# Kernel tuning notes

Measured on AMD Instinct MI355X. Metric: run time of the kernel, lower is better.

## Reference

```python
import jax, jax.numpy as jnp
import numpy as np

L, H = 6, 8          # depth, heads
DM, DH, M = 512, 64, 256  # d_model, d_head, nb random features
EPS = 1e-4


def sinusoidal_pe(n, d, dtype):
    pos = jnp.arange(n, dtype=jnp.float32)[:, None]
    div = jnp.exp(jnp.arange(0, d, 2, dtype=jnp.float32) * (-(np.log(10000.0) / d)))
    pe = jnp.zeros((n, d), jnp.float32)
    pe = pe.at[:, 0::2].set(jnp.sin(pos * div))
    pe = pe.at[:, 1::2].set(jnp.cos(pos * div))
    return pe.astype(dtype)


def layer_norm(x, g, b, eps=1e-5):
    mu = jnp.mean(x, -1, keepdims=True)
    var = jnp.mean(jnp.square(x - mu), -1, keepdims=True)
    return (x - mu) * jax.lax.rsqrt(var + eps) * g + b


def softmax_features(x, proj, is_query):
    # FAVOR+ positive softmax-kernel features. x: [b,h,n,dh], proj: [m,dh]
    dn = DH ** -0.25
    xd = x * dn
    u = jnp.einsum('bhnd,md->bhnm', xd, proj)            # [b,h,n,m]
    diag = 0.5 * jnp.sum(xd * xd, -1, keepdims=True)      # ||x||^2/2 (normalized)
    if is_query:
        stab = jnp.max(u, axis=-1, keepdims=True)
    else:
        stab = jnp.max(u, axis=(-2, -1), keepdims=True)
    return (M ** -0.5) * (jnp.exp(u - diag - stab) + EPS)


def split_heads(t, b, n):
    return t.reshape(b, n, H, DH).transpose(0, 2, 1, 3)   # [b,h,n,dh]


def reference(x, proj, ln1_g, ln1_b, wq, wk, wv, wo, bo, ln2_g, ln2_b, w1, b1, w2, b2):
    b, n, d = x.shape
    x = x + sinusoidal_pe(n, d, x.dtype)[None]
    for i in range(L):
        # --- FAVOR+ linear attention (pre-norm) ---
        h = layer_norm(x, ln1_g[i], ln1_b[i])
        q = split_heads(h @ wq[i], b, n)
        k = split_heads(h @ wk[i], b, n)
        v = split_heads(h @ wv[i], b, n)
        qp = softmax_features(q, proj[i], True)           # [b,h,n,m]
        kp = softmax_features(k, proj[i], False)
        ksum = jnp.sum(kp, axis=2)                         # [b,h,m]
        d_inv = 1.0 / jnp.einsum('bhnm,bhm->bhn', qp, ksum)
        ctx = jnp.einsum('bhnm,bhnd->bhmd', kp, v)         # [b,h,m,dh]
        o = jnp.einsum('bhnm,bhmd->bhnd', qp, ctx) * d_inv[..., None]
        o = o.transpose(0, 2, 1, 3).reshape(b, n, DM)
        x = x + o @ wo[i] + bo[i]
        # --- feed-forward (pre-norm, GELU) ---
        h = layer_norm(x, ln2_g[i], ln2_b[i])
        x = x + jax.nn.gelu(h @ w1[i] + b1[i], approximate=False) @ w2[i] + b2[i]
    return x


def setup_inputs() -> dict:
    key = jax.random.key(0)
    ks = jax.random.split(key, 9)
    s_in = DM ** -0.5
    s_ff = (4 * DM) ** -0.5
    return {
        'x':     jax.random.normal(ks[0], (8, 2048, DM), jnp.float32),
        'proj':  jax.random.normal(ks[1], (L, M, DH), jnp.float32),
        'ln1_g': jnp.ones((L, DM), jnp.float32),
        'ln1_b': jnp.zeros((L, DM), jnp.float32),
        'wq':    jax.random.normal(ks[2], (L, DM, DM), jnp.float32) * s_in,
        'wk':    jax.random.normal(ks[3], (L, DM, DM), jnp.float32) * s_in,
        'wv':    jax.random.normal(ks[4], (L, DM, DM), jnp.float32) * s_in,
        'wo':    jax.random.normal(ks[5], (L, DM, DM), jnp.float32) * s_in,
        'bo':    jnp.zeros((L, DM), jnp.float32),
        'ln2_g': jnp.ones((L, DM), jnp.float32),
        'ln2_b': jnp.zeros((L, DM), jnp.float32),
        'w1':    jax.random.normal(ks[6], (L, DM, 4 * DM), jnp.float32) * s_in,
        'b1':    jnp.zeros((L, 4 * DM), jnp.float32),
        'w2':    jax.random.normal(ks[7], (L, 4 * DM, DM), jnp.float32) * s_ff,
        'b2':    jnp.zeros((L, DM), jnp.float32),
    }
```

## Files before the change

kernel.cpp:

```cpp
#include <hip/hip_runtime.h>
#include <math.h>

#define LNUM 6
#define HNUM 8
#define DMODEL 512
#define DHEAD 64
#define MFEAT 256
#define BATCH 8
#define SEQ 2048
#define TOK (BATCH*SEQ)
#define BHN (BATCH*HNUM)
#define DFF 2048
#define EPSF 1e-4f
#define LN_EPS 1e-5f
#define DNRM 0.35355339059327373f
#define SMF 0.0625f

typedef unsigned short u16;
typedef __attribute__((ext_vector_type(8))) short bf16x8;
typedef __attribute__((ext_vector_type(4))) float f32x4;
#define MFMA16(a,b,c) __builtin_amdgcn_mfma_f32_16x16x32_bf16(a,b,c,0,0,0)

#define GLOAD16(g,l) __builtin_amdgcn_global_load_lds( \
    (const __attribute__((address_space(1))) void*)(g), \
    (__attribute__((address_space(3))) void*)(l), 16, 0, 0)

__device__ __forceinline__ u16 f2bf(float f){
  unsigned int u = __float_as_uint(f);
  u = (u + 0x7fffu + ((u >> 16) & 1u)) >> 16;
  return (u16)u;
}
__device__ __forceinline__ float bf2f(u16 s){
  return __uint_as_float(((unsigned int)s) << 16);
}
__device__ __forceinline__ void atomicMaxF(float* addr, float val){
  if(val >= 0.f) atomicMax((int*)addr, __float_as_int(val));
  else           atomicMin((unsigned int*)addr, __float_as_uint(val));
}
__device__ __forceinline__ float fast_gelu(float z){
  float g2 = z*(1.5957691216f + 0.07135481628f*z*z);
  return z / (1.0f + __expf(-g2));
}

__global__ void k_addpe(const float* __restrict__ x, float* __restrict__ xo){
  int idx = blockIdx.x*256 + threadIdx.x;
  int d = idx & (DMODEL-1);
  int n = (idx >> 9) & (SEQ-1);
  int j = d >> 1;
  float freq = expf((float)(2*j) * (-9.210340371976184f / (float)DMODEL));
  float ang = (float)n * freq;
  float pe = (d & 1) ? cosf(ang) : sinf(ang);
  xo[idx] = x[idx] + pe;
}

__global__ void k_ln(const float* __restrict__ x, const float* __restrict__ g,
                     const float* __restrict__ bv, u16* __restrict__ out){
  __shared__ float sred[8];
  int t = blockIdx.x, tid = threadIdx.x;
  const float2 v = ((const float2*)(x + (size_t)t*DMODEL))[tid];
  float s = v.x + v.y;
  #pragma unroll
  for(int o=32;o;o>>=1) s += __shfl_down(s,o);
  if((tid&63)==0) sred[tid>>6] = s;
  __syncthreads();
  if(tid==0) sred[4] = (sred[0]+sred[1]+sred[2]+sred[3]) * (1.0f/DMODEL);
  __syncthreads();
  float mu = sred[4];
  float dx = v.x - mu, dy = v.y - mu;
  float s2 = dx*dx + dy*dy;
  #pragma unroll
  for(int o=32;o;o>>=1) s2 += __shfl_down(s2,o);
  if((tid&63)==0) sred[tid>>6] = s2;
  __syncthreads();
  if(tid==0) sred[5] = rsqrtf((sred[0]+sred[1]+sred[2]+sred[3])*(1.0f/DMODEL) + LN_EPS);
  __syncthreads();
  float rs = sred[5];
  const float2 gg = ((const float2*)g)[tid];
  const float2 bb = ((const float2*)bv)[tid];
  ushort2 o2; o2.x = f2bf(dx*rs*gg.x + bb.x); o2.y = f2bf(dy*rs*gg.y + bb.y);
  ((ushort2*)(out + (size_t)t*DMODEL))[tid] = o2;
}

__global__ void k_pcvt(const float* __restrict__ p, u16* __restrict__ pb){
  int i = blockIdx.x*256 + threadIdx.x;
  pb[i] = f2bf(p[i]);
}

__global__ void k_wcvt_all(const float* __restrict__ wq, const float* __restrict__ wk,
                           const float* __restrict__ wv, const float* __restrict__ wo,
                           const float* __restrict__ w1, const float* __restrict__ w2,
                           u16* __restrict__ wqT, u16* __restrict__ wkT,
                           u16* __restrict__ wvT, u16* __restrict__ woT,
                           u16* __restrict__ w1T, u16* __restrict__ w2T,
                           float* __restrict__ ksum, float* __restrict__ kmax){
  int bid = blockIdx.x;
  if(bid >= 768){
    int i = (bid-768)*256 + threadIdx.x;
    ksum[i] = 0.f;
    if(i < BHN) kmax[i] = -INFINITY;
    return;
  }
  const float* src; u16* dst; int K, N, bx, by;
  if(bid < 256){
    int which = bid >> 6, sub = bid & 63;
    src = which==0 ? wq : which==1 ? wk : which==2 ? wv : wo;
    dst = which==0 ? wqT : which==1 ? wkT : which==2 ? wvT : woT;
    K = 512; N = 512; bx = sub & 7; by = sub >> 3;
  } else if(bid < 512){
    int sub = bid - 256; src = w1; dst = w1T; K = 512; N = 2048; bx = sub & 31; by = sub >> 5;
  } else {
    int sub = bid - 512; src = w2; dst = w2T; K = 2048; N = 512; bx = sub & 7; by = sub >> 3;
  }
  __shared__ float sm[64][65];
  int kt = by*64, nt = bx*64;
  int t = threadIdx.x, c = t & 63, r4 = t >> 6;
  #pragma unroll
  for(int i=0;i<16;i++){
    int kl = i*4 + r4;
    sm[kl][c] = src[(size_t)(kt+kl)*N + nt + c];
  }
  __syncthreads();
  #pragma unroll
  for(int i=0;i<16;i++){
    int nl = i*4 + r4;
    dst[(size_t)(nt+nl)*K + kt + c] = f2bf(sm[c][nl]);
  }
}

template<int EPI>
__global__ __launch_bounds__(256,4)
void k_mm(const u16* __restrict__ A, const u16* __restrict__ Bt,
          const float* __restrict__ bias, void* __restrict__ Cv,
          int Nc, int K){
  __shared__ u16 As[2][128*32];
  __shared__ u16 Bs[2][128*32];
  int tid = threadIdx.x;
  int w = tid >> 6, lane = tid & 63;
  int wr = w >> 1, wc = w & 1;
  int hi = lane >> 4, li = lane & 15;
  int row0 = blockIdx.y*128, col0 = blockIdx.x*128;
  int lr = lane >> 2;
  int cs = (lane & 3) ^ ((lane >> 3) & 3);
  const u16* gA = A  + (size_t)(row0 + w*16 + lr)*K + cs*8;
  const u16* gB = Bt + (size_t)(col0 + w*16 + lr)*K + cs*8;
  int rb = li*32 + ((hi ^ ((li>>1)&3))<<3);
  f32x4 acc[4][4] = {};

#define STAGE_MM(b,k0) { \
    GLOAD16(gA + (k0),                &As[b][(w*16)*32]);      \
    GLOAD16(gA + (size_t)64*K + (k0), &As[b][(64+w*16)*32]);   \
    GLOAD16(gB + (k0),                &Bs[b][(w*16)*32]);      \
    GLOAD16(gB + (size_t)64*K + (k0), &Bs[b][(64+w*16)*32]); }

  int nk = K >> 5;
  STAGE_MM(0, 0)
  STAGE_MM(1, 32)
  for(int t=0; t<nk; ++t){
    __builtin_amdgcn_sched_barrier(0);
    if(t+1 < nk){ asm volatile("s_waitcnt vmcnt(4)"); }
    else        { asm volatile("s_waitcnt vmcnt(0)"); }
    __builtin_amdgcn_s_barrier();
    __builtin_amdgcn_sched_barrier(0);
    const u16* pa = &As[t&1][0];
    const u16* pb = &Bs[t&1][0];
    bf16x8 bfr[4];
    #pragma unroll
    for(int q=0;q<4;q++) bfr[q] = *(const bf16x8*)&pb[rb + wc*2048 + q*512];
    #pragma unroll
    for(int i2=0;i2<4;i2++){
      bf16x8 a = *(const bf16x8*)&pa[rb + wr*2048 + i2*512];
      #pragma unroll
      for(int j2=0;j2<4;j2++)
        acc[i2][j2] = MFMA16(a, bfr[j2], acc[i2][j2]);
    }
    __builtin_amdgcn_sched_barrier(0);
    __builtin_amdgcn_s_barrier();
    __builtin_amdgcn_sched_barrier(0);
    if(t+2 < nk){ STAGE_MM(t&1, (size_t)(t+2)*32) }
  }
#undef STAGE_MM

  #pragma unroll
  for(int i2=0;i2<4;i2++){
    #pragma unroll
    for(int j2=0;j2<4;j2++){
      int col = col0 + wc*64 + j2*16 + li;
      float bcol = (EPI==2 || EPI==3) ? bias[col] : 0.f;
      if constexpr (EPI==4){
        int nb = row0 + wr*64 + i2*16 + hi*4;
        int b = nb >> 11, n = nb & (SEQ-1);
        int h = col >> 6, dh = col & 63;
        ushort4 pk;
        pk.x = f2bf(acc[i2][j2][0]); pk.y = f2bf(acc[i2][j2][1]);
        pk.z = f2bf(acc[i2][j2][2]); pk.w = f2bf(acc[i2][j2][3]);
        *(ushort4*)((u16*)Cv + (((size_t)(b*HNUM+h)*DHEAD + dh)*SEQ + n)) = pk;
      } else {
        #pragma unroll
        for(int r=0;r<4;r++){
          int row = row0 + wr*64 + i2*16 + hi*4 + r;
          float v = acc[i2][j2][r];
          if constexpr (EPI==1){
            int b = row >> 11, n = row & (SEQ-1);
            int h = col >> 6, dh = col & 63;
            ((u16*)Cv)[((size_t)(b*HNUM+h)*SEQ + n)*DHEAD + dh] = f2bf(v);
          } else if constexpr (EPI==2){
            ((float*)Cv)[(size_t)row*Nc + col] += v + bcol;
          } else {
            ((u16*)Cv)[(size_t)row*Nc + col] = f2bf(fast_gelu(v + bcol));
          }
        }
      }
    }
  }
}

__global__ __launch_bounds__(256)
void k_kmax(const u16* __restrict__ xg, const u16* __restrict__ pjb,
            float* __restrict__ kmax){
  __shared__ u16 pj[256*64];
  __shared__ u16 xs[128*64];
  __shared__ float wred[4];
  int tid = threadIdx.x, w = tid >> 6, lane = tid & 63;
  int hi = lane >> 4, li = lane & 15;
  int r0 = blockIdx.x * 128;
  int bh = r0 >> 11;
  #pragma unroll
  for(int i=0;i<8;i++){
    int idx = i*256 + tid;
    int m = idx >> 3, c = idx & 7;
    bf16x8 v = *(const bf16x8*)(pjb + m*64 + c*8);
    *(bf16x8*)&pj[m*64 + ((c ^ (m&7))<<3)] = v;
  }
  #pragma unroll
  for(int i=0;i<4;i++){
    int idx = i*256 + tid;
    int m = idx >> 3, c = idx & 7;
    bf16x8 v = *(const bf16x8*)(xg + (size_t)(r0+m)*64 + c*8);
    *(bf16x8*)&xs[m*64 + ((c ^ (m&7))<<3)] = v;
  }
  __syncthreads();
  bf16x8 bfr[2][4];
  #pragma unroll
  for(int ks=0;ks<2;ks++){
    int kc = ks*4 + hi;
    #pragma unroll
    for(int t=0;t<4;t++){
      int bc = w*64 + t*16 + li;
      bfr[ks][t] = *(const bf16x8*)&pj[bc*64 + ((kc ^ (bc&7))<<3)];
    }
  }
  float mx = -1e30f;
  #pragma unroll
  for(int i8=0;i8<8;i8++){
    f32x4 acc[4] = {};
    #pragma unroll
    for(int ks=0;ks<2;ks++){
      int kc = ks*4 + hi;
      int ar = i8*16 + li;
      bf16x8 af = *(const bf16x8*)&xs[ar*64 + ((kc ^ (ar&7))<<3)];
      #pragma unroll
      for(int j2=0;j2<4;j2++)
        acc[j2] = MFMA16(af, bfr[ks][j2], acc[j2]);
    }
    #pragma unroll
    for(int j2=0;j2<4;j2++)
      #pragma unroll
      for(int r=0;r<4;r++) mx = fmaxf(mx, acc[j2][r]);
  }
  #pragma unroll
  for(int o=32;o;o>>=1) mx = fmaxf(mx, __shfl_xor(mx,o));
  if(lane==0) wred[w] = mx;
  __syncthreads();
  if(tid==0){
    float m2 = fmaxf(fmaxf(wred[0],wred[1]), fmaxf(wred[2],wred[3]));
    atomicMaxF(&kmax[bh], m2*DNRM);
  }
}

__global__ __launch_bounds__(256)
void k_kfeat(const u16* __restrict__ xg, const u16* __restrict__ pjb,
             u16* __restrict__ outp, const float* __restrict__ kmax,
             float* __restrict__ ksum){
  __shared__ u16 pj[256*64];
  __shared__ u16 xs[128*64];
  __shared__ float dgs[128];
  int tid = threadIdx.x, w = tid >> 6, lane = tid & 63;
  int hi = lane >> 4, li = lane & 15;
  int r0 = blockIdx.x * 128;
  int bh = r0 >> 11;
  int nbase = r0 & (SEQ-1);
  #pragma unroll
  for(int i=0;i<8;i++){
    int idx = i*256 + tid;
    int m = idx >> 3, c = idx & 7;
    bf16x8 v = *(const bf16x8*)(pjb + m*64 + c*8);
    *(bf16x8*)&pj[m*64 + ((c ^ (m&7))<<3)] = v;
  }
  #pragma unroll
  for(int i=0;i<4;i++){
    int idx = i*256 + tid;
    int m = idx >> 3, c = idx & 7;
    bf16x8 v = *(const bf16x8*)(xg + (size_t)(r0+m)*64 + c*8);
    *(bf16x8*)&xs[m*64 + ((c ^ (m&7))<<3)] = v;
    float s = 0.f;
    #pragma unroll
    for(int j=0;j<8;j++){ float t = bf2f((u16)v[j]); s += t*t; }
    s += __shfl_xor(s,1); s += __shfl_xor(s,2); s += __shfl_xor(s,4);
    if((tid&7)==0) dgs[m] = 0.5f*DNRM*DNRM*s;
  }
  __syncthreads();
  bf16x8 bfr[2][4];
  #pragma unroll
  for(int ks=0;ks<2;ks++){
    int kc = ks*4 + hi;
    #pragma unroll
    for(int t=0;t<4;t++){
      int bc = w*64 + t*16 + li;
      bfr[ks][t] = *(const bf16x8*)&pj[bc*64 + ((kc ^ (bc&7))<<3)];
    }
  }
  float km = kmax[bh];
  float csum[4] = {0.f,0.f,0.f,0.f};
  #pragma unroll
  for(int i8=0;i8<8;i8++){
    f32x4 acc[4] = {};
    #pragma unroll
    for(int ks=0;ks<2;ks++){
      int kc = ks*4 + hi;
      int ar = i8*16 + li;
      bf16x8 af = *(const bf16x8*)&xs[ar*64 + ((kc ^ (ar&7))<<3)];
      #pragma unroll
      for(int j2=0;j2<4;j2++)
        acc[j2] = MFMA16(af, bfr[ks][j2], acc[j2]);
    }
    #pragma unroll
    for(int j2=0;j2<4;j2++){
      int col = w*64 + j2*16 + li;
      ushort4 pk;
      float cpart = 0.f;
      #pragma unroll
      for(int r=0;r<4;r++){
        int rl = i8*16 + hi*4 + r;
        float u = acc[j2][r]*DNRM;
        u16 eb = f2bf(SMF*(__expf(u - dgs[rl] - km) + EPSF));
        ((u16*)&pk)[r] = eb;
        cpart += bf2f(eb);
      }
      *(ushort4*)(outp + ((size_t)(bh*MFEAT + col)*SEQ + nbase + i8*16 + hi*4)) = pk;
      csum[j2] += cpart;
    }
  }
  #pragma unroll
  for(int j2=0;j2<4;j2++){
    float v = csum[j2];
    v += __shfl_xor(v,16); v += __shfl_xor(v,32);
    if(hi==0) atomicAdd(&ksum[bh*MFEAT + w*64 + j2*16 + li], v);
  }
}

__global__ __launch_bounds__(512)
void k_feato(const u16* __restrict__ xg, const u16* __restrict__ pjb,
             const u16* __restrict__ ctxt, const float* __restrict__ ksum,
             u16* __restrict__ o){
  __shared__ u16 smA[16384];
  __shared__ u16 smX[4096];
  __shared__ u16 smQ[64*264];
  __shared__ float dgs[64];
  __shared__ float wred[2][4][32];
  __shared__ float wden[2][4][32];
  __shared__ float ksl[256];
  __shared__ float denl[64];
  int tid = threadIdx.x, w = tid >> 6, lane = tid & 63;
  int hi = lane >> 4, li = lane & 15;
  int g = w >> 2, wq = w & 3;
  int r0 = blockIdx.x * 64;
  int bh = r0 >> 11;
  int b = bh >> 3, h = bh & 7;
  #pragma unroll
  for(int i=0;i<4;i++){
    int idx = i*512 + tid;
    int m = idx >> 3, c = idx & 7;
    bf16x8 v = *(const bf16x8*)(pjb + m*64 + c*8);
    *(bf16x8*)&smA[m*64 + ((c ^ (m&7))<<3)] = v;
  }
  {
    int m = tid >> 3, c = tid & 7;
    bf16x8 v = *(const bf16x8*)(xg + (size_t)(r0+m)*64 + c*8);
    *(bf16x8*)&smX[m*64 + ((c ^ (m&7))<<3)] = v;
    float s = 0.f;
    #pragma unroll
    for(int j=0;j<8;j++){ float t = bf2f((u16)v[j]); s += t*t; }
    s += __shfl_xor(s,1); s += __shfl_xor(s,2); s += __shfl_xor(s,4);
    if((tid&7)==0) dgs[m] = 0.5f*DNRM*DNRM*s;
  }
  if(tid < 256) ksl[tid] = ksum[bh*MFEAT + tid];
  __syncthreads();
  f32x4 acc[2][4] = {};
  #pragma unroll
  for(int ks=0;ks<2;ks++){
    bf16x8 af[2], bfr[4];
    int kc = ks*4 + hi;
    #pragma unroll
    for(int t=0;t<2;t++){
      int ar = g*32 + t*16 + li;
      af[t] = *(const bf16x8*)&smX[ar*64 + ((kc ^ (ar&7))<<3)];
    }
    #pragma unroll
    for(int t=0;t<4;t++){
      int bc = wq*64 + t*16 + li;
      bfr[t] = *(const bf16x8*)&smA[bc*64 + ((kc ^ (bc&7))<<3)];
    }
    #pragma unroll
    for(int i2=0;i2<2;i2++)
      #pragma unroll
      for(int j2=0;j2<4;j2++)
        acc[i2][j2] = MFMA16(af[i2], bfr[j2], acc[i2][j2]);
  }
  __syncthreads();
  {
    int gch = (tid & 31) ^ ((tid >> 5) & 7);
    const u16* gCl = ctxt + (size_t)bh*DHEAD*MFEAT + (size_t)(tid>>5)*MFEAT + gch*8;
    #pragma unroll
    for(int i=0;i<4;i++)
      GLOAD16(gCl + (size_t)i*16*MFEAT, &smA[i*4096 + w*512]);
  }
  #pragma unroll
  for(int i2=0;i2<2;i2++){
    #pragma unroll
    for(int r=0;r<4;r++){
      float v = fmaxf(fmaxf(acc[i2][0][r],acc[i2][1][r]), fmaxf(acc[i2][2][r],acc[i2][3][r]));
      v = fmaxf(v, __shfl_xor(v,1)); v = fmaxf(v, __shfl_xor(v,2));
      v = fmaxf(v, __shfl_xor(v,4)); v = fmaxf(v, __shfl_xor(v,8));
      if(li==0) wred[g][wq][i2*16 + hi*4 + r] = v;
    }
  }
  __builtin_amdgcn_sched_barrier(0);
  asm volatile("s_waitcnt lgkmcnt(0)");
  __builtin_amdgcn_s_barrier();
  __builtin_amdgcn_sched_barrier(0);
  #pragma unroll
  for(int i2=0;i2<2;i2++){
    #pragma unroll
    for(int r=0;r<4;r++){
      int rl = i2*16 + hi*4 + r;
      int row = g*32 + rl;
      float rm = fmaxf(fmaxf(wred[g][0][rl],wred[g][1][rl]),
                       fmaxf(wred[g][2][rl],wred[g][3][rl]));
      float dsum = 0.f;
      #pragma unroll
      for(int j2=0;j2<4;j2++){
        int col = wq*64 + j2*16 + li;
        float u = acc[i2][j2][r]*DNRM;
        u16 eb = f2bf(SMF*(__expf(u - dgs[row] - rm) + EPSF));
        smQ[row*264 + col] = eb;
        dsum += bf2f(eb)*ksl[col];
      }
      dsum += __shfl_xor(dsum,1); dsum += __shfl_xor(dsum,2);
      dsum += __shfl_xor(dsum,4); dsum += __shfl_xor(dsum,8);
      if(li==0) wden[g][wq][rl] = dsum;
    }
  }
  __builtin_amdgcn_sched_barrier(0);
  asm volatile("s_waitcnt vmcnt(0) lgkmcnt(0)");
  __builtin_amdgcn_s_barrier();
  __builtin_amdgcn_sched_barrier(0);
  if(tid < 64){
    int gg = tid >> 5, rr = tid & 31;
    denl[tid] = wden[gg][0][rr]+wden[gg][1][rr]+wden[gg][2][rr]+wden[gg][3][rr];
  }
  int d4 = w >> 1, g2 = w & 1;
  f32x4 acc2[2] = {};
  #pragma unroll
  for(int s=0;s<8;s++){
    int kc = s*4 + hi;
    int bc = d4*16 + li;
    bf16x8 bf = *(const bf16x8*)&smA[bc*256 + ((kc ^ (bc&7))<<3)];
    #pragma unroll
    for(int t=0;t<2;t++){
      int ar = g2*32 + t*16 + li;
      bf16x8 aa = *(const bf16x8*)&smQ[ar*264 + kc*8];
      acc2[t] = MFMA16(aa, bf, acc2[t]);
    }
  }
  __syncthreads();
  int nbase = r0 & (SEQ-1);
  #pragma unroll
  for(int t=0;t<2;t++){
    #pragma unroll
    for(int r=0;r<4;r++){
      int nl = g2*32 + t*16 + hi*4 + r;
      float di = 1.0f/denl[nl];
      o[((size_t)b*SEQ + nbase + nl)*DMODEL + h*DHEAD + d4*16 + li] = f2bf(acc2[t][r]*di);
    }
  }
}

__global__ __launch_bounds__(256)
void k_ctx(const u16* __restrict__ vt, const u16* __restrict__ kpt,
           u16* __restrict__ ctxt){
  __shared__ u16 As[2][64*64];
  __shared__ u16 Bs[2][64*64];
  int tid = threadIdx.x, w = tid >> 6, lane = tid & 63;
  int wr = w >> 1, wc = w & 1;
  int hi = lane >> 4, li = lane & 15;
  int bh = blockIdx.y, mb = blockIdx.x*64;
  int lr = lane >> 3;
  int lc = (lane & 7) ^ lr;
  const u16* gA = vt  + (size_t)bh*DHEAD*SEQ + (size_t)(w*8 + lr)*SEQ + lc*8;
  const u16* gB = kpt + ((size_t)bh*MFEAT + mb + w*8 + lr)*SEQ + lc*8;
  f32x4 acc[2][2] = {};
#define STAGE_CTX(b,k0) { \
    GLOAD16(gA + (k0),                 &As[b][(w*8)*64]);      \
    GLOAD16(gA + (size_t)32*SEQ + (k0),&As[b][(32+w*8)*64]);   \
    GLOAD16(gB + (k0),                 &Bs[b][(w*8)*64]);      \
    GLOAD16(gB + (size_t)32*SEQ + (k0),&Bs[b][(32+w*8)*64]); }
  int nk = SEQ/64;
  STAGE_CTX(0, 0)
  STAGE_CTX(1, 64)
  for(int t=0; t<nk; ++t){
    __builtin_amdgcn_sched_barrier(0);
    if(t+1 < nk){ asm volatile("s_waitcnt vmcnt(4)"); }
    else        { asm volatile("s_waitcnt vmcnt(0)"); }
    __builtin_amdgcn_s_barrier();
    __builtin_amdgcn_sched_barrier(0);
    const u16* pa = &As[t&1][0];
    const u16* pb = &Bs[t&1][0];
    #pragma unroll
    for(int ks=0;ks<2;ks++){
      bf16x8 af[2], bfr[2];
      int kc = ks*4 + hi;
      #pragma unroll
      for(int q=0;q<2;q++){
        int ar = wr*32 + q*16 + li;
        af[q] = *(const bf16x8*)&pa[ar*64 + ((kc ^ (ar&7))<<3)];
        int bc = wc*32 + q*16 + li;
        bfr[q] = *(const bf16x8*)&pb[bc*64 + ((kc ^ (bc&7))<<3)];
      }
      #pragma unroll
      for(int i2=0;i2<2;i2++)
        #pragma unroll
        for(int j2=0;j2<2;j2++)
          acc[i2][j2] = MFMA16(af[i2], bfr[j2], acc[i2][j2]);
    }
    __builtin_amdgcn_sched_barrier(0);
    __builtin_amdgcn_s_barrier();
    __builtin_amdgcn_sched_barrier(0);
    if(t+2 < nk){ STAGE_CTX(t&1, (size_t)(t+2)*64) }
  }
#undef STAGE_CTX
  #pragma unroll
  for(int i2=0;i2<2;i2++)
    #pragma unroll
    for(int j2=0;j2<2;j2++){
      int m = mb + wc*32 + j2*16 + li;
      #pragma unroll
      for(int r=0;r<4;r++){
        int dh = wr*32 + i2*16 + hi*4 + r;
        ctxt[((size_t)bh*DHEAD + dh)*MFEAT + m] = f2bf(acc[i2][j2][r]);
      }
    }
}

extern "C" void kernel_launch(void* const* d_in, const int* in_sizes, int n_in,
                              void* d_out, int out_size, void* d_ws, size_t ws_size,
                              hipStream_t stream){
  (void)in_sizes; (void)n_in; (void)out_size; (void)ws_size;
  const float* x    = (const float*)d_in[0];
  const float* proj = (const float*)d_in[1];
  const float* ln1g = (const float*)d_in[2];
  const float* ln1b = (const float*)d_in[3];
  const float* wq   = (const float*)d_in[4];
  const float* wk   = (const float*)d_in[5];
  const float* wv   = (const float*)d_in[6];
  const float* wo   = (const float*)d_in[7];
  const float* bo   = (const float*)d_in[8];
  const float* ln2g = (const float*)d_in[9];
  const float* ln2b = (const float*)d_in[10];
  const float* w1   = (const float*)d_in[11];
  const float* b1   = (const float*)d_in[12];
  const float* w2   = (const float*)d_in[13];
  const float* b2   = (const float*)d_in[14];
  float* xo = (float*)d_out;

  char* ws = (char*)d_ws;
  u16* bufH  = (u16*)ws;  ws += (size_t)TOK*DMODEL*2;
  u16* bufA  = (u16*)ws;  ws += (size_t)TOK*DMODEL*2;
  u16* featb = (u16*)ws;  ws += (size_t)BHN*SEQ*MFEAT*2;
  u16* ctxt  = (u16*)ws;  ws += (size_t)BHN*DHEAD*MFEAT*2;
  u16* wT    = (u16*)ws;  ws += (size_t)3*1048576*2;
  u16* pjb   = (u16*)ws;  ws += (size_t)LNUM*MFEAT*DHEAD*2;
  float* ksum= (float*)ws; ws += (size_t)BHN*MFEAT*4;
  float* kmax= (float*)ws; ws += 256;

  u16* wqT = wT;
  u16* wkT = wT +  262144;
  u16* wvT = wT +  524288;
  u16* woT = wT +  786432;
  u16* w1T = wT + 1048576;
  u16* w2T = wT + 2097152;

  k_addpe<<<(TOK*DMODEL)/256, 256, 0, stream>>>(x, xo);
  k_pcvt<<<(LNUM*MFEAT*DHEAD)/256, 256, 0, stream>>>(proj, pjb);

  for(int l=0; l<LNUM; l++){
    const u16* pj_l = pjb + (size_t)l*MFEAT*DHEAD;
    k_wcvt_all<<<832, 256, 0, stream>>>(wq + (size_t)l*262144, wk + (size_t)l*262144,
                                        wv + (size_t)l*262144, wo + (size_t)l*262144,
                                        w1 + (size_t)l*1048576, w2 + (size_t)l*1048576,
                                        wqT, wkT, wvT, woT, w1T, w2T, ksum, kmax);
    k_ln<<<TOK, 256, 0, stream>>>(xo, ln1g + l*DMODEL, ln1b + l*DMODEL, bufH);
    k_mm<1><<<dim3(4,128), 256, 0, stream>>>(bufH, wkT, nullptr, bufA, DMODEL, DMODEL);
    k_kmax<<<(BHN*SEQ)/128, 256, 0, stream>>>(bufA, pj_l, kmax);
    k_kfeat<<<(BHN*SEQ)/128, 256, 0, stream>>>(bufA, pj_l, featb, kmax, ksum);
    k_mm<4><<<dim3(4,128), 256, 0, stream>>>(bufH, wvT, nullptr, bufA, DMODEL, DMODEL);
    k_ctx<<<dim3(4,BHN), 256, 0, stream>>>(bufA, featb, ctxt);
    k_mm<1><<<dim3(4,128), 256, 0, stream>>>(bufH, wqT, nullptr, bufA, DMODEL, DMODEL);
    k_feato<<<(BHN*SEQ)/64, 512, 0, stream>>>(bufA, pj_l, ctxt, ksum, bufH);
    k_mm<2><<<dim3(4,128), 256, 0, stream>>>(bufH, woT, bo + l*DMODEL, xo, DMODEL, DMODEL);
    k_ln<<<TOK, 256, 0, stream>>>(xo, ln2g + l*DMODEL, ln2b + l*DMODEL, bufA);
    k_mm<3><<<dim3(16,128), 256, 0, stream>>>(bufA, w1T, b1 + l*DFF, featb, DFF, DMODEL);
    k_mm<2><<<dim3(4,128), 256, 0, stream>>>(featb, w2T, b2 + l*DMODEL, xo, DMODEL, DFF);
  }
}
```

Measured before the change: 2.079 ms.

## Replace GEMM with 256x128 tile, 8-wave, triple-buffered K=64 pipeline

The bf16 GEMM kernel is rebuilt to use 512-thread blocks computing 256x128 output tiles with a K-step of 64. A three-stage LDS ring buffer holds the tiles, using an XOR swizzle for bank-conflict-free reads. Global-to-LDS loads for stage t+2 are interleaved between two MFMA halves, and s_setprio raises priority around the MFMA bursts. The aim is more reuse per LDS load and better overlap of memory with compute, at the cost of higher LDS use (about 144KB) and fewer blocks per CU.

```diff
diff --git a/kernel.cpp b/kernel.cpp
--- a/kernel.cpp
+++ b/kernel.cpp
@@ -128,57 +128,102 @@
 }
 
 template<int EPI>
-__global__ __launch_bounds__(256,4)
-void k_mm(const u16* __restrict__ A, const u16* __restrict__ Bt,
-          const float* __restrict__ bias, void* __restrict__ Cv,
-          int Nc, int K){
-  __shared__ u16 As[2][128*32];
-  __shared__ u16 Bs[2][128*32];
+__global__ __launch_bounds__(512)
+void k_mm8(const u16* __restrict__ A, const u16* __restrict__ Bt,
+           const float* __restrict__ bias, void* __restrict__ Cv,
+           int Nc, int K){
+  __shared__ u16 Ab[3][256*64];
+  __shared__ u16 Bb[3][128*64];
   int tid = threadIdx.x;
   int w = tid >> 6, lane = tid & 63;
   int wr = w >> 1, wc = w & 1;
   int hi = lane >> 4, li = lane & 15;
-  int row0 = blockIdx.y*128, col0 = blockIdx.x*128;
-  int lr = lane >> 2;
-  int cs = (lane & 3) ^ ((lane >> 3) & 3);
-  const u16* gA = A  + (size_t)(row0 + w*16 + lr)*K + cs*8;
-  const u16* gB = Bt + (size_t)(col0 + w*16 + lr)*K + cs*8;
-  int rb = li*32 + ((hi ^ ((li>>1)&3))<<3);
+  int row0 = blockIdx.y*256, col0 = blockIdx.x*128;
+  int lr = lane >> 3;
+  int lc = (lane & 7) ^ lr;
+  const u16* gA = A  + (size_t)(row0 + w*8 + lr)*K + lc*8;
+  const u16* gB = Bt + (size_t)(col0 + w*8 + lr)*K + lc*8;
   f32x4 acc[4][4] = {};
 
-#define STAGE_MM(b,k0) { \
-    GLOAD16(gA + (k0),                &As[b][(w*16)*32]);      \
-    GLOAD16(gA + (size_t)64*K + (k0), &As[b][(64+w*16)*32]);   \
-    GLOAD16(gB + (k0),                &Bs[b][(w*16)*32]);      \
-    GLOAD16(gB + (size_t)64*K + (k0), &Bs[b][(64+w*16)*32]); }
-
-  int nk = K >> 5;
-  STAGE_MM(0, 0)
-  STAGE_MM(1, 32)
+#define STG8(buf,k0) { \
+    GLOAD16(gA + (k0),                  &Ab[buf][w*512]);          \
+    GLOAD16(gA + (size_t)64*K  + (k0),  &Ab[buf][4096  + w*512]);  \
+    GLOAD16(gA + (size_t)128*K + (k0),  &Ab[buf][8192  + w*512]);  \
+    GLOAD16(gA + (size_t)192*K + (k0),  &Ab[buf][12288 + w*512]);  \
+    GLOAD16(gB + (k0),                  &Bb[buf][w*512]);          \
+    GLOAD16(gB + (size_t)64*K  + (k0),  &Bb[buf][4096  + w*512]); }
+
+  int nk = K >> 6;
+  STG8(0, 0)
+  STG8(1, 64)
   for(int t=0; t<nk; ++t){
+    int buf = t % 3;
+    int nbuf = (t+2) % 3;
+    size_t nk0 = (size_t)(t+2)*64;
     __builtin_amdgcn_sched_barrier(0);
-    if(t+1 < nk){ asm volatile("s_waitcnt vmcnt(4)"); }
+    if(t+1 < nk){ asm volatile("s_waitcnt vmcnt(6)"); }
     else        { asm volatile("s_waitcnt vmcnt(0)"); }
     __builtin_amdgcn_s_barrier();
     __builtin_amdgcn_sched_barrier(0);
-    const u16* pa = &As[t&1][0];
-    const u16* pb = &Bs[t&1][0];
-    bf16x8 bfr[4];
-    #pragma unroll
-    for(int q=0;q<4;q++) bfr[q] = *(const bf16x8*)&pb[rb + wc*2048 + q*512];
-    #pragma unroll
-    for(int i2=0;i2<4;i2++){
-      bf16x8 a = *(const bf16x8*)&pa[rb + wr*2048 + i2*512];
-      #pragma unroll
-      for(int j2=0;j2<4;j2++)
-        acc[i2][j2] = MFMA16(a, bfr[j2], acc[i2][j2]);
-    }
-    __builtin_amdgcn_sched_barrier(0);
+    const u16* pa = &Ab[buf][0];
+    const u16* pb = &Bb[buf][0];
+    bf16x8 bfr[2][4], af[2][2];
+    #pragma unroll
+    for(int kk=0;kk<2;kk++){
+      int kc = kk*4 + hi;
+      #pragma unroll
+      for(int j=0;j<4;j++){
+        int bc = wc*64 + j*16 + li;
+        bfr[kk][j] = *(const bf16x8*)&pb[bc*64 + ((kc ^ (bc&7))<<3)];
+      }
+      #pragma unroll
+      for(int q=0;q<2;q++){
+        int ar = wr*64 + q*16 + li;
+        af[kk][q] = *(const bf16x8*)&pa[ar*64 + ((kc ^ (ar&7))<<3)];
+      }
+    }
+    if(t+2 < nk){
+      GLOAD16(gA + nk0,                  &Ab[nbuf][w*512]);
+      GLOAD16(gA + (size_t)64*K  + nk0,  &Ab[nbuf][4096  + w*512]);
+      GLOAD16(gA + (size_t)128*K + nk0,  &Ab[nbuf][8192  + w*512]);
+    }
+    __builtin_amdgcn_s_setprio(1);
+    #pragma unroll
+    for(int kk=0;kk<2;kk++)
+      #pragma unroll
+      for(int q=0;q<2;q++)
+        #pragma unroll
+        for(int j=0;j<4;j++)
+          acc[q][j] = MFMA16(af[kk][q], bfr[kk][j], acc[q][j]);
+    __builtin_amdgcn_s_setprio(0);
     __builtin_amdgcn_s_barrier();
-    __builtin_amdgcn_sched_barrier(0);
-    if(t+2 < nk){ STAGE_MM(t&1, (size_t)(t+2)*32) }
-  }
-#undef STAGE_MM
+    bf16x8 af2[2][2];
+    #pragma unroll
+    for(int kk=0;kk<2;kk++){
+      int kc = kk*4 + hi;
+      #pragma unroll
+      for(int q=0;q<2;q++){
+        int ar = wr*64 + (q+2)*16 + li;
+        af2[kk][q] = *(const bf16x8*)&pa[ar*64 + ((kc ^ (ar&7))<<3)];
+      }
+    }
+    if(t+2 < nk){
+      GLOAD16(gA + (size_t)192*K + nk0,  &Ab[nbuf][12288 + w*512]);
+      GLOAD16(gB + nk0,                  &Bb[nbuf][w*512]);
+      GLOAD16(gB + (size_t)64*K  + nk0,  &Bb[nbuf][4096  + w*512]);
+    }
+    __builtin_amdgcn_s_setprio(1);
+    #pragma unroll
+    for(int kk=0;kk<2;kk++)
+      #pragma unroll
+      for(int q=0;q<2;q++)
+        #pragma unroll
+        for(int j=0;j<4;j++)
+          acc[q+2][j] = MFMA16(af2[kk][q], bfr[kk][j], acc[q+2][j]);
+    __builtin_amdgcn_s_setprio(0);
+    __builtin_amdgcn_s_barrier();
+  }
+#undef STG8
 
   #pragma unroll
   for(int i2=0;i2<4;i2++){
@@ -609,16 +654,16 @@
                                         w1 + (size_t)l*1048576, w2 + (size_t)l*1048576,
                                         wqT, wkT, wvT, woT, w1T, w2T, ksum, kmax);
     k_ln<<<TOK, 256, 0, stream>>>(xo, ln1g + l*DMODEL, ln1b + l*DMODEL, bufH);
-    k_mm<1><<<dim3(4,128), 256, 0, stream>>>(bufH, wkT, nullptr, bufA, DMODEL, DMODEL);
+    k_mm8<1><<<dim3(4,64), 512, 0, stream>>>(bufH, wkT, nullptr, bufA, DMODEL, DMODEL);
     k_kmax<<<(BHN*SEQ)/128, 256, 0, stream>>>(bufA, pj_l, kmax);
     k_kfeat<<<(BHN*SEQ)/128, 256, 0, stream>>>(bufA, pj_l, featb, kmax, ksum);
-    k_mm<4><<<dim3(4,128), 256, 0, stream>>>(bufH, wvT, nullptr, bufA, DMODEL, DMODEL);
+    k_mm8<4><<<dim3(4,64), 512, 0, stream>>>(bufH, wvT, nullptr, bufA, DMODEL, DMODEL);
     k_ctx<<<dim3(4,BHN), 256, 0, stream>>>(bufA, featb, ctxt);
-    k_mm<1><<<dim3(4,128), 256, 0, stream>>>(bufH, wqT, nullptr, bufA, DMODEL, DMODEL);
+    k_mm8<1><<<dim3(4,64), 512, 0, stream>>>(bufH, wqT, nullptr, bufA, DMODEL, DMODEL);
     k_feato<<<(BHN*SEQ)/64, 512, 0, stream>>>(bufA, pj_l, ctxt, ksum, bufH);
-    k_mm<2><<<dim3(4,128), 256, 0, stream>>>(bufH, woT, bo + l*DMODEL, xo, DMODEL, DMODEL);
+    k_mm8<2><<<dim3(4,64), 512, 0, stream>>>(bufH, woT, bo + l*DMODEL, xo, DMODEL, DMODEL);
     k_ln<<<TOK, 256, 0, stream>>>(xo, ln2g + l*DMODEL, ln2b + l*DMODEL, bufA);
-    k_mm<3><<<dim3(16,128), 256, 0, stream>>>(bufA, w1T, b1 + l*DFF, featb, DFF, DMODEL);
-    k_mm<2><<<dim3(4,128), 256, 0, stream>>>(featb, w2T, b2 + l*DMODEL, xo, DMODEL, DFF);
-  }
-}
+    k_mm8<3><<<dim3(16,64), 512, 0, stream>>>(bufA, w1T, b1 + l*DFF, featb, DFF, DMODEL);
+    k_mm8<2><<<dim3(4,64), 512, 0, stream>>>(featb, w2T, b2 + l*DMODEL, xo, DMODEL, DFF);
+  }
+}
```

After: 2.043 ms. About the same (-1.7%).
